# Kernel optimization log

Hardware: AMD Instinct MI355X
Metric: run time of the kernel (lower is better)

Reference implementation:

```python
import jax, jax.numpy as jnp
import numpy as np
import math

B, L, D, H = 2, 4096, 1024, 16
DH = D // H


def _build_table(seq_len):
    # Faithful port of build_hierarchical_index_lookup_table (static, host-side).
    assert seq_len & (seq_len - 1) == 0
    levels = int(math.log2(seq_len))
    max_valid = 2 * seq_len - 3
    idx = np.full((seq_len, levels), -1, dtype=np.int64)
    cm = np.zeros((seq_len, levels), dtype=bool)
    for n in range(seq_len):
        c = n
        for lvl in range(levels):
            if lvl == 0:
                nxt = c ^ 1
                pair = c
            else:
                nxt = (c // 2 + seq_len) ^ 1
                pair = c // 2 + seq_len
            if nxt > max_valid:
                break
            if pair < nxt:
                cm[n, lvl] = True
            idx[n, lvl] = nxt
            c = nxt
    return idx, cm


def setup_inputs() -> dict:
    rng = jax.random.key(0)
    ks = jax.random.split(rng, 8)
    s = 0.02  # init scale for weights
    idx, cm = _build_table(L)
    return {
        "query": jax.random.normal(ks[0], (B, L, D), jnp.float32),
        "key": jax.random.normal(ks[1], (B, L, D), jnp.float32),
        "value": jax.random.normal(ks[2], (B, L, D), jnp.float32),
        "Wq": jax.random.normal(ks[3], (D, D), jnp.float32) * s,
        "Wk": jax.random.normal(ks[4], (D, D), jnp.float32) * s,
        "Wv": jax.random.normal(ks[5], (D, D), jnp.float32) * s,
        "Wo": jax.random.normal(ks[6], (D, D), jnp.float32) * s,
        "bo": jax.random.normal(ks[7], (D,), jnp.float32) * s,
        "idx_table": jnp.asarray(idx),        # [L, log2(L)] int64
        "causal_mask": jnp.asarray(cm),       # [L, log2(L)] bool
    }


def reference(query, key, value, Wq, Wk, Wv, Wo, bo, idx_table, causal_mask):
    Bq, Lq, Dm = query.shape
    scale = 1.0 / math.sqrt(DH)

    def heads(x, W):  # nn.Linear (no bias) + split heads -> [B,H,L,Dh]
        return (x @ W.T).reshape(Bq, Lq, H, DH).transpose(0, 2, 1, 3)

    Q = heads(query, Wq)
    K = heads(key, Wk)
    V = heads(value, Wv)

    # Build binary-tree hierarchy. Pair weights come from softmax of ZERO
    # logits (Q_parent starts as zeros in the source), so w0 = w1 = 0.5 exactly.
    Ks, Vs = [K], [V]
    while Ks[-1].shape[2] > 1:
        k, v = Ks[-1], Vs[-1]
        Lc = k.shape[2]
        k2 = k.reshape(Bq, H, Lc // 2, 2, DH)
        v2 = v.reshape(Bq, H, Lc // 2, 2, DH)
        Ks.append(0.5 * (k2[:, :, :, 0] + k2[:, :, :, 1]))
        Vs.append(v2[:, :, :, 0] + v2[:, :, :, 1])
    flatK = jnp.concatenate(Ks, axis=2)  # [B,H,2L-1,Dh]
    flatV = jnp.concatenate(Vs, axis=2)

    # Gather neighbor nodes across levels: [B,H,L,levels,Dh]
    nk = flatK[:, :, idx_table]
    nv = flatV[:, :, idx_table]

    self_logits = jnp.einsum('bhnd,bhnd->bhn', Q, K) * scale
    nbr_logits = jnp.einsum('bhld,bhlnd->bhln', Q, nk) * scale
    nbr_logits = jnp.where(causal_mask[None, None], -jnp.inf, nbr_logits)

    all_logits = jnp.concatenate([self_logits[..., None], nbr_logits], axis=-1)
    w = jax.nn.softmax(all_logits, axis=-1)           # [B,H,L,1+levels]
    all_v = jnp.concatenate([V[:, :, :, None, :], nv], axis=3)
    out = jnp.einsum('bhln,bhlnd->bhld', w, all_v)    # [B,H,L,Dh]
    out = out.transpose(0, 2, 1, 3).reshape(Bq, Lq, Dm)
    return out @ Wo.T + bo
```

## Files before the change

kernel.cpp:

```cpp
#include <hip/hip_runtime.h>
#include <cstdint>
#include <cstddef>


typedef __bf16 bf16;
typedef __bf16 bf16x8 __attribute__((ext_vector_type(8)));
typedef __bf16 bf16x4 __attribute__((ext_vector_type(4)));
typedef float  f32x4  __attribute__((ext_vector_type(4)));

#define L_SEQ  4096
#define NFLAT  8192

__device__ __forceinline__ int off_l(int l) { return 8192 - (8192 >> l); }

__device__ __forceinline__ void glds16(const bf16* g, bf16* l) {
  __builtin_amdgcn_global_load_lds(
      (const __attribute__((address_space(1))) unsigned int*)g,
      (__attribute__((address_space(3))) unsigned int*)l, 16, 0, 0);
}

#define MEMFENCE asm volatile("" ::: "memory")
__device__ __forceinline__ void barrier_raw() {
  MEMFENCE; __builtin_amdgcn_s_barrier(); MEMFENCE;
}

__device__ __forceinline__ int swz(int b) { return b ^ (((b >> 9) & 1) << 5); }
__device__ __forceinline__ int la(int row, int col) {
  return ((((row >> 4) << 1) + (col >> 5)) << 10) + ((row & 15) << 6) + ((col & 31) << 1);
}

__global__ __launch_bounds__(256) void cvt3_kernel(
    const float* __restrict__ a, const float* __restrict__ b, const float* __restrict__ c,
    bf16* __restrict__ x, bf16* __restrict__ y, bf16* __restrict__ z) {
  const int s = blockIdx.y;
  const float* src = (s == 0) ? a : (s == 1) ? b : c;
  bf16*        dst = (s == 0) ? x : (s == 1) ? y : z;
  const int i = blockIdx.x * 256 + threadIdx.x;
  const float4 v = ((const float4*)src)[i];
  bf16x4 o;
  o[0] = (bf16)v.x; o[1] = (bf16)v.y; o[2] = (bf16)v.z; o[3] = (bf16)v.w;
  *(bf16x4*)(dst + (size_t)i * 4) = o;
}

__global__ __launch_bounds__(256) void cvt4_kernel(
    const float* __restrict__ a, const float* __restrict__ b,
    const float* __restrict__ c, const float* __restrict__ d,
    bf16* __restrict__ x, bf16* __restrict__ y, bf16* __restrict__ z, bf16* __restrict__ w) {
  const int s = blockIdx.y;
  const float* src = (s == 0) ? a : (s == 1) ? b : (s == 2) ? c : d;
  bf16*        dst = (s == 0) ? x : (s == 1) ? y : (s == 2) ? z : w;
  const int i = blockIdx.x * 256 + threadIdx.x;
  const float4 v = ((const float4*)src)[i];
  bf16x4 o;
  o[0] = (bf16)v.x; o[1] = (bf16)v.y; o[2] = (bf16)v.z; o[3] = (bf16)v.w;
  *(bf16x4*)(dst + (size_t)i * 4) = o;
}

#define BUFB 32768

__device__ __forceinline__ void stage_tile(const bf16* __restrict__ A,
                                           const bf16* __restrict__ W,
                                           int tm, int tn, int k0,
                                           char* buf, int tid, int wid) {
  bf16* Ad = (bf16*)buf;
  bf16* Bd = (bf16*)(buf + 16384);
#pragma unroll
  for (int i = 0; i < 4; i++) {
    const int d  = i * 4096 + tid * 16;
    const int lb = swz(d);
    const int row = ((lb >> 10) >> 1) * 16 + ((lb >> 6) & 15);
    const int col = ((lb >> 10) & 1) * 32 + ((lb & 63) >> 1);
    glds16(A + (size_t)(tm * 128 + row) * 1024 + k0 + col, Ad + ((i * 4096 + wid * 1024) >> 1));
    glds16(W + (size_t)(tn * 128 + row) * 1024 + k0 + col, Bd + ((i * 4096 + wid * 1024) >> 1));
  }
}

__device__ __forceinline__ void gemm8_core(const bf16* __restrict__ A,
                                           const bf16* __restrict__ W,
                                           int tm, int tn, char* lds,
                                           f32x4 (&acc)[4][4]) {
  const int tid  = threadIdx.x;
  const int wid  = tid >> 6, lane = tid & 63;
  const int wm   = wid >> 1, wn = wid & 1;
  const int laneR  = lane & 15;
  const int laneC8 = (lane >> 4) * 8;

  stage_tile(A, W, tm, tn, 0, lds, tid, wid);

  for (int u = 0; u < 16; ++u) {
    asm volatile("s_waitcnt vmcnt(0)" ::: "memory");
    barrier_raw();
    if (u + 1 < 16)
      stage_tile(A, W, tm, tn, (u + 1) << 6, lds + ((u + 1) & 1) * BUFB, tid, wid);

    const char* Ab = lds + (u & 1) * BUFB;
    const char* Bb = Ab + 16384;
    bf16x8 af[4][2], bfr[4][2];
#pragma unroll
    for (int f = 0; f < 4; f++)
#pragma unroll
      for (int ks = 0; ks < 2; ks++)
        af[f][ks] = *(const bf16x8*)(Ab + swz(la(wm * 64 + f * 16 + laneR, ks * 32 + laneC8)));
#pragma unroll
    for (int j = 0; j < 4; j++)
#pragma unroll
      for (int ks = 0; ks < 2; ks++)
        bfr[j][ks] = *(const bf16x8*)(Bb + swz(la(wn * 64 + j * 16 + laneR, ks * 32 + laneC8)));

    __builtin_amdgcn_s_setprio(1);
#pragma unroll
    for (int f = 0; f < 4; f++)
#pragma unroll
      for (int j = 0; j < 4; j++)
#pragma unroll
        for (int ks = 0; ks < 2; ks++)
          acc[f][j] = __builtin_amdgcn_mfma_f32_16x16x32_bf16(
              af[f][ks], bfr[j][ks], acc[f][j], 0, 0, 0);
    __builtin_amdgcn_s_setprio(0);
  }
}

__device__ __forceinline__ void tile_map(int bid, int& tm, int& tn) {
  const int xcd = bid & 7, q = bid >> 3;
  tm = xcd * 8 + (q >> 3);
  tn = q & 7;
}

__global__ __launch_bounds__(256, 2) void gemm8_qkv_kernel(
    const bf16* __restrict__ qx, const bf16* __restrict__ kx, const bf16* __restrict__ vx,
    const bf16* __restrict__ wq, const bf16* __restrict__ wk, const bf16* __restrict__ wv,
    bf16* __restrict__ Qb, bf16* __restrict__ fK, bf16* __restrict__ fV) {
  __shared__ __align__(16) char lds[2 * BUFB];
  const int z = blockIdx.y;
  const bf16* A = (z == 0) ? qx : (z == 1) ? kx : vx;
  const bf16* W = (z == 0) ? wq : (z == 1) ? wk : wv;
  bf16* D       = (z == 0) ? Qb : (z == 1) ? fK : fV;
  const int lstr = (z == 0) ? L_SEQ : NFLAT;
  int tm, tn; tile_map(blockIdx.x, tm, tn);
  f32x4 acc[4][4] = {};
  gemm8_core(A, W, tm, tn, lds, acc);
  const int lane = threadIdx.x & 63, wid = threadIdx.x >> 6;
  const int m0 = tm * 128 + (wid >> 1) * 64 + (lane >> 4) * 4;
  const int n0 = tn * 128 + (wid & 1) * 64 + (lane & 15);
#pragma unroll
  for (int i = 0; i < 4; i++)
#pragma unroll
    for (int j = 0; j < 4; j++)
#pragma unroll
      for (int r = 0; r < 4; r++) {
        const int m = m0 + i * 16 + r;
        const int n = n0 + j * 16;
        const int b = m >> 12, l = m & 4095;
        const int h = n >> 6,  dh = n & 63;
        D[((size_t)(b * 16 + h) * lstr + l) * 64 + dh] = (bf16)acc[i][j][r];
      }
}

__global__ __launch_bounds__(256, 2) void gemm8_out_kernel(
    const bf16* __restrict__ Ob, const bf16* __restrict__ wo,
    const float* __restrict__ bo, float* __restrict__ out) {
  __shared__ __align__(16) char lds[2 * BUFB];
  int tm, tn; tile_map(blockIdx.x, tm, tn);
  f32x4 acc[4][4] = {};
  gemm8_core(Ob, wo, tm, tn, lds, acc);
  const int lane = threadIdx.x & 63, wid = threadIdx.x >> 6;
  const int m0 = tm * 128 + (wid >> 1) * 64 + (lane >> 4) * 4;
  const int n0 = tn * 128 + (wid & 1) * 64 + (lane & 15);
#pragma unroll
  for (int i = 0; i < 4; i++)
#pragma unroll
    for (int j = 0; j < 4; j++)
#pragma unroll
      for (int r = 0; r < 4; r++) {
        const int m = m0 + i * 16 + r;
        const int n = n0 + j * 16;
        out[(size_t)m * 1024 + n] = acc[i][j][r] + bo[n];
      }
}

__global__ __launch_bounds__(64) void tree_l16(bf16* __restrict__ fK, bf16* __restrict__ fV) {
  __shared__ __align__(16) bf16 Kl[64 * 64];
  __shared__ __align__(16) bf16 Vl[64 * 64];
  const int g = blockIdx.x, bh = blockIdx.y;
  const int lane = threadIdx.x;
  const size_t fb = (size_t)bh * NFLAT * 64;
  const size_t leafbase = fb + (size_t)g * 64 * 64;
#pragma unroll
  for (int it = 0; it < 8; it++) {
    glds16(fK + leafbase + it * 512 + lane * 8, Kl + it * 512);
    glds16(fV + leafbase + it * 512 + lane * 8, Vl + it * 512);
  }
  asm volatile("s_waitcnt vmcnt(0)" ::: "memory");
  __syncthreads();

  float pk[7], pv[7];
#pragma unroll
  for (int i = 0; i < 64; i++) {
    float ck = (float)Kl[i * 64 + lane];
    float cv = (float)Vl[i * 64 + lane];
#pragma unroll
    for (int l = 1; l <= 6; l++) {
      if (((i + 1) & ((1 << l) - 1)) != 0) { pk[l] = ck; pv[l] = cv; break; }
      ck += pk[l]; cv += pv[l];
      const int j = (g * 64 + i) >> l;
      fK[fb + (size_t)(off_l(l) + j) * 64 + lane] = (bf16)(ck * (1.0f / (1 << l)));
      fV[fb + (size_t)(off_l(l) + j) * 64 + lane] = (bf16)cv;
    }
  }
}

__global__ __launch_bounds__(64) void tree_l712(bf16* __restrict__ fK, bf16* __restrict__ fV) {
  __shared__ float Ks[64 * 64];
  __shared__ float Vs[64 * 64];
  const int bh = blockIdx.x, d = threadIdx.x;
  const size_t fb = (size_t)bh * NFLAT * 64;
#pragma unroll 8
  for (int i = 0; i < 64; i++) {
    Ks[i * 64 + d] = (float)fK[fb + (size_t)(8064 + i) * 64 + d];
    Vs[i * 64 + d] = (float)fV[fb + (size_t)(8064 + i) * 64 + d];
  }
#pragma unroll
  for (int l = 7; l <= 12; l++) {
    const int cnt = 4096 >> l;
    for (int j = 0; j < cnt; j++) {
      const float k = (Ks[(2 * j) * 64 + d] + Ks[(2 * j + 1) * 64 + d]) * 0.5f;
      const float v =  Vs[(2 * j) * 64 + d] + Vs[(2 * j + 1) * 64 + d];
      Ks[j * 64 + d] = k;
      Vs[j * 64 + d] = v;
      fK[fb + (size_t)(off_l(l) + j) * 64 + d] = (bf16)k;
      fV[fb + (size_t)(off_l(l) + j) * 64 + d] = (bf16)v;
    }
  }
}

__global__ __launch_bounds__(64) void attn_kernel(
    const bf16* __restrict__ Qb, const bf16* __restrict__ fK,
    const bf16* __restrict__ fV, bf16* __restrict__ Ob) {
  __shared__ __align__(16) unsigned short Kl[132 * 64];
  __shared__ __align__(16) unsigned short Vl[132 * 64];
  const int t0  = blockIdx.x * 64;
  const int bh  = blockIdx.y;
  const int tid = threadIdx.x;
  const size_t fb = (size_t)bh * NFLAT * 64;

  for (int u = tid; u < 132 * 8; u += 64) {
    const int r = u >> 3, c = u & 7;
    int flat;
    if      (r < 64)  flat = t0 + r;
    else if (r < 96)  flat = 4096 + (t0 >> 1) + (r - 64);
    else if (r < 112) flat = 6144 + (t0 >> 2) + (r - 96);
    else if (r < 120) flat = 7168 + (t0 >> 3) + (r - 112);
    else if (r < 124) flat = 7680 + (t0 >> 4) + (r - 120);
    else if (r < 126) flat = 7936 + (t0 >> 5) + (r - 124);
    else { const int l = r - 120; flat = (8192 - (8192 >> l) + (t0 >> l)) ^ 1; }
    const int cc = c ^ (r & 7);
    const uint4 kk = *(const uint4*)((const char*)(fK + fb + (size_t)flat * 64) + c * 16);
    const uint4 vv = *(const uint4*)((const char*)(fV + fb + (size_t)flat * 64) + c * 16);
    *(uint4*)((char*)Kl + r * 128 + cc * 16) = kk;
    *(uint4*)((char*)Vl + r * 128 + cc * 16) = vv;
  }
  __syncthreads();

  const int n = t0 + tid;
  int rows[13];
  rows[0] = tid;
#pragma unroll
  for (int l = 0; l < 12; l++) {
    int r;
    if (l == 0)      r = tid ^ 1;
    else if (l <= 5) r = (128 - (128 >> l)) + (((n >> l) ^ 1) - (t0 >> l));
    else             r = 126 + (l - 6);
    rows[l + 1] = r;
  }

  float q[64];
  const bf16* Qr = Qb + ((size_t)bh * L_SEQ + n) * 64;
#pragma unroll
  for (int c = 0; c < 8; c++) {
    bf16x8 v = *(const bf16x8*)(Qr + c * 8);
#pragma unroll
    for (int j = 0; j < 8; j++) q[c * 8 + j] = (float)v[j];
  }

  float lg[13];
#pragma unroll
  for (int v = 0; v < 13; v++) {
    const int r = rows[v];
    float a = 0.f;
#pragma unroll
    for (int c = 0; c < 8; c++) {
      const int cc = c ^ (r & 7);
      const bf16x8 kv = *(const bf16x8*)((const char*)Kl + r * 128 + cc * 16);
#pragma unroll
      for (int j = 0; j < 8; j++) a += q[c * 8 + j] * (float)kv[j];
    }
    lg[v] = a * 0.125f;
  }
#pragma unroll
  for (int v = 1; v < 13; v++)
    if (!((n >> (v - 1)) & 1)) lg[v] = -1e30f;

  float mx = lg[0];
#pragma unroll
  for (int v = 1; v < 13; v++) mx = fmaxf(mx, lg[v]);
  float w[13], s = 0.f;
#pragma unroll
  for (int v = 0; v < 13; v++) { w[v] = __expf(lg[v] - mx); s += w[v]; }
  const float inv = 1.0f / s;

  float o[64];
#pragma unroll
  for (int d = 0; d < 64; d++) o[d] = 0.f;
#pragma unroll
  for (int v = 0; v < 13; v++) {
    const int r = rows[v];
    const float wv = w[v];
#pragma unroll
    for (int c = 0; c < 8; c++) {
      const int cc = c ^ (r & 7);
      const bf16x8 vv = *(const bf16x8*)((const char*)Vl + r * 128 + cc * 16);
#pragma unroll
      for (int j = 0; j < 8; j++) o[c * 8 + j] += wv * (float)vv[j];
    }
  }

  bf16* Or = Ob + ((size_t)(bh >> 4) * L_SEQ + n) * 1024 + (size_t)(bh & 15) * 64;
#pragma unroll
  for (int c = 0; c < 8; c++) {
    bf16x8 ov;
#pragma unroll
    for (int j = 0; j < 8; j++) ov[j] = (bf16)(o[c * 8 + j] * inv);
    *(bf16x8*)(Or + c * 8) = ov;
  }
}

extern "C" void kernel_launch(void* const* d_in, const int* in_sizes, int n_in,
                              void* d_out, int out_size, void* d_ws, size_t ws_size,
                              hipStream_t stream) {
  const float* query = (const float*)d_in[0];
  const float* key   = (const float*)d_in[1];
  const float* value = (const float*)d_in[2];
  const float* Wq    = (const float*)d_in[3];
  const float* Wk    = (const float*)d_in[4];
  const float* Wv    = (const float*)d_in[5];
  const float* Wo    = (const float*)d_in[6];
  const float* bo    = (const float*)d_in[7];
  float* out = (float*)d_out;

  char* ws = (char*)d_ws;
  size_t off = 0;
  auto take = [&](size_t bytes) -> void* {
    void* p = ws + off;
    off += (bytes + 255) & ~(size_t)255;
    return p;
  };
  const size_t XB = (size_t)8192 * 1024 * 2;
  const size_t WB = (size_t)1024 * 1024 * 2;
  bf16* qx  = (bf16*)take(XB);
  bf16* kx  = (bf16*)take(XB);
  bf16* vx  = (bf16*)take(XB);
  bf16* wqx = (bf16*)take(WB);
  bf16* wkx = (bf16*)take(WB);
  bf16* wvx = (bf16*)take(WB);
  bf16* wox = (bf16*)take(WB);
  bf16* Qb  = (bf16*)take((size_t)32 * L_SEQ * 64 * 2);
  bf16* fK  = (bf16*)take((size_t)32 * NFLAT * 64 * 2);
  bf16* fV  = (bf16*)take((size_t)32 * NFLAT * 64 * 2);
  bf16* Ob  = qx;
  (void)in_sizes; (void)n_in; (void)out_size; (void)ws_size;

  cvt3_kernel<<<dim3(8192, 3), 256, 0, stream>>>(query, key, value, qx, kx, vx);
  cvt4_kernel<<<dim3(1024, 4), 256, 0, stream>>>(Wq, Wk, Wv, Wo, wqx, wkx, wvx, wox);

  gemm8_qkv_kernel<<<dim3(512, 3), 256, 0, stream>>>(qx, kx, vx, wqx, wkx, wvx, Qb, fK, fV);

  tree_l16 <<<dim3(64, 32), 64, 0, stream>>>(fK, fV);
  tree_l712<<<32, 64, 0, stream>>>(fK, fV);

  attn_kernel<<<dim3(64, 32), 64, 0, stream>>>(Qb, fK, fV, Ob);

  gemm8_out_kernel<<<512, 256, 0, stream>>>(Ob, wox, bo, out);
}
```

Before: 165.3 us.

## Fuse tree levels 1-6 into QKV GEMM epilogue and merge convert kernels

```diff
diff --git a/kernel.cpp b/kernel.cpp
--- a/kernel.cpp
+++ b/kernel.cpp
@@ -29,30 +29,28 @@
   return ((((row >> 4) << 1) + (col >> 5)) << 10) + ((row & 15) << 6) + ((col & 31) << 1);
 }
 
-__global__ __launch_bounds__(256) void cvt3_kernel(
-    const float* __restrict__ a, const float* __restrict__ b, const float* __restrict__ c,
-    bf16* __restrict__ x, bf16* __restrict__ y, bf16* __restrict__ z) {
-  const int s = blockIdx.y;
-  const float* src = (s == 0) ? a : (s == 1) ? b : c;
-  bf16*        dst = (s == 0) ? x : (s == 1) ? y : z;
-  const int i = blockIdx.x * 256 + threadIdx.x;
-  const float4 v = ((const float4*)src)[i];
+__global__ __launch_bounds__(256) void cvtall_kernel(
+    const float* __restrict__ q, const float* __restrict__ k, const float* __restrict__ v,
+    const float* __restrict__ wq, const float* __restrict__ wk,
+    const float* __restrict__ wv, const float* __restrict__ wo,
+    bf16* __restrict__ qx, bf16* __restrict__ kx, bf16* __restrict__ vx,
+    bf16* __restrict__ wqx, bf16* __restrict__ wkx, bf16* __restrict__ wvx,
+    bf16* __restrict__ wox) {
+  const int y = blockIdx.y;
+  int i = blockIdx.x * 256 + threadIdx.x;
+  const float* src; bf16* dst;
+  if (y < 3) {
+    src = (y == 0) ? q : (y == 1) ? k : v;
+    dst = (y == 0) ? qx : (y == 1) ? kx : vx;
+  } else {
+    if (i >= 1048576) return;
+    const int w = i >> 18; i &= 262143;
+    src = (w == 0) ? wq : (w == 1) ? wk : (w == 2) ? wv : wo;
+    dst = (w == 0) ? wqx : (w == 1) ? wkx : (w == 2) ? wvx : wox;
+  }
+  const float4 t = ((const float4*)src)[i];
   bf16x4 o;
-  o[0] = (bf16)v.x; o[1] = (bf16)v.y; o[2] = (bf16)v.z; o[3] = (bf16)v.w;
-  *(bf16x4*)(dst + (size_t)i * 4) = o;
-}
-
-__global__ __launch_bounds__(256) void cvt4_kernel(
-    const float* __restrict__ a, const float* __restrict__ b,
-    const float* __restrict__ c, const float* __restrict__ d,
-    bf16* __restrict__ x, bf16* __restrict__ y, bf16* __restrict__ z, bf16* __restrict__ w) {
-  const int s = blockIdx.y;
-  const float* src = (s == 0) ? a : (s == 1) ? b : (s == 2) ? c : d;
-  bf16*        dst = (s == 0) ? x : (s == 1) ? y : (s == 2) ? z : w;
-  const int i = blockIdx.x * 256 + threadIdx.x;
-  const float4 v = ((const float4*)src)[i];
-  bf16x4 o;
-  o[0] = (bf16)v.x; o[1] = (bf16)v.y; o[2] = (bf16)v.z; o[3] = (bf16)v.w;
+  o[0] = (bf16)t.x; o[1] = (bf16)t.y; o[2] = (bf16)t.z; o[3] = (bf16)t.w;
   *(bf16x4*)(dst + (size_t)i * 4) = o;
 }
 
@@ -139,21 +137,55 @@
   int tm, tn; tile_map(blockIdx.x, tm, tn);
   f32x4 acc[4][4] = {};
   gemm8_core(A, W, tm, tn, lds, acc);
+
   const int lane = threadIdx.x & 63, wid = threadIdx.x >> 6;
-  const int m0 = tm * 128 + (wid >> 1) * 64 + (lane >> 4) * 4;
-  const int n0 = tn * 128 + (wid & 1) * 64 + (lane & 15);
+  const int rl0 = (wid >> 1) * 64 + (lane >> 4) * 4;
+  const int cl0 = (wid & 1) * 64 + (lane & 15);
 #pragma unroll
   for (int i = 0; i < 4; i++)
 #pragma unroll
     for (int j = 0; j < 4; j++)
 #pragma unroll
       for (int r = 0; r < 4; r++) {
-        const int m = m0 + i * 16 + r;
-        const int n = n0 + j * 16;
+        const int m = tm * 128 + rl0 + i * 16 + r;
+        const int n = tn * 128 + cl0 + j * 16;
         const int b = m >> 12, l = m & 4095;
         const int h = n >> 6,  dh = n & 63;
         D[((size_t)(b * 16 + h) * lstr + l) * 64 + dh] = (bf16)acc[i][j][r];
       }
+
+  if (z != 0) {
+    bf16* Ct = (bf16*)lds;
+    barrier_raw();
+#pragma unroll
+    for (int i = 0; i < 4; i++)
+#pragma unroll
+      for (int j = 0; j < 4; j++)
+#pragma unroll
+        for (int r = 0; r < 4; r++)
+          Ct[(rl0 + i * 16 + r) * 132 + (cl0 + j * 16)] = (bf16)acc[i][j][r];
+    barrier_raw();
+
+    const int g2 = threadIdx.x >> 7;
+    const int c  = threadIdx.x & 127;
+    const int h  = tn * 2 + (c >> 6), dh = c & 63;
+    const int b  = (tm * 128) >> 12;
+    const int lbase = ((tm * 128) & 4095) + g2 * 64;
+    const size_t fb = (size_t)(b * 16 + h) * NFLAT * 64 + dh;
+    float pk[7];
+#pragma unroll
+    for (int i = 0; i < 64; i++) {
+      float ck = (float)Ct[(g2 * 64 + i) * 132 + c];
+#pragma unroll
+      for (int l = 1; l <= 6; l++) {
+        if (((i + 1) & ((1 << l) - 1)) != 0) { pk[l] = ck; break; }
+        ck += pk[l];
+        const int j = (lbase + i) >> l;
+        D[fb + (size_t)(off_l(l) + j) * 64] =
+            (bf16)(z == 1 ? ck * (1.0f / (1 << l)) : ck);
+      }
+    }
+  }
 }
 
 __global__ __launch_bounds__(256, 2) void gemm8_out_kernel(
@@ -176,37 +208,6 @@
         const int n = n0 + j * 16;
         out[(size_t)m * 1024 + n] = acc[i][j][r] + bo[n];
       }
-}
-
-__global__ __launch_bounds__(64) void tree_l16(bf16* __restrict__ fK, bf16* __restrict__ fV) {
-  __shared__ __align__(16) bf16 Kl[64 * 64];
-  __shared__ __align__(16) bf16 Vl[64 * 64];
-  const int g = blockIdx.x, bh = blockIdx.y;
-  const int lane = threadIdx.x;
-  const size_t fb = (size_t)bh * NFLAT * 64;
-  const size_t leafbase = fb + (size_t)g * 64 * 64;
-#pragma unroll
-  for (int it = 0; it < 8; it++) {
-    glds16(fK + leafbase + it * 512 + lane * 8, Kl + it * 512);
-    glds16(fV + leafbase + it * 512 + lane * 8, Vl + it * 512);
-  }
-  asm volatile("s_waitcnt vmcnt(0)" ::: "memory");
-  __syncthreads();
-
-  float pk[7], pv[7];
-#pragma unroll
-  for (int i = 0; i < 64; i++) {
-    float ck = (float)Kl[i * 64 + lane];
-    float cv = (float)Vl[i * 64 + lane];
-#pragma unroll
-    for (int l = 1; l <= 6; l++) {
-      if (((i + 1) & ((1 << l) - 1)) != 0) { pk[l] = ck; pv[l] = cv; break; }
-      ck += pk[l]; cv += pv[l];
-      const int j = (g * 64 + i) >> l;
-      fK[fb + (size_t)(off_l(l) + j) * 64 + lane] = (bf16)(ck * (1.0f / (1 << l)));
-      fV[fb + (size_t)(off_l(l) + j) * 64 + lane] = (bf16)cv;
-    }
-  }
 }
 
 __global__ __launch_bounds__(64) void tree_l712(bf16* __restrict__ fK, bf16* __restrict__ fV) {
@@ -369,12 +370,11 @@
   bf16* Ob  = qx;
   (void)in_sizes; (void)n_in; (void)out_size; (void)ws_size;
 
-  cvt3_kernel<<<dim3(8192, 3), 256, 0, stream>>>(query, key, value, qx, kx, vx);
-  cvt4_kernel<<<dim3(1024, 4), 256, 0, stream>>>(Wq, Wk, Wv, Wo, wqx, wkx, wvx, wox);
+  cvtall_kernel<<<dim3(8192, 4), 256, 0, stream>>>(
+      query, key, value, Wq, Wk, Wv, Wo, qx, kx, vx, wqx, wkx, wvx, wox);
 
   gemm8_qkv_kernel<<<dim3(512, 3), 256, 0, stream>>>(qx, kx, vx, wqx, wkx, wvx, Qb, fK, fV);
 
-  tree_l16 <<<dim3(64, 32), 64, 0, stream>>>(fK, fV);
   tree_l712<<<32, 64, 0, stream>>>(fK, fV);
 
   attn_kernel<<<dim3(64, 32), 64, 0, stream>>>(Qb, fK, fV, Ob);
```

Result: faster. 160.9 us (-2.6%).
